# Kernel tuning notes

Measured on AMD Instinct MI355X. Metric: run time of the kernel, lower is better.

Reference implementation:

```python
import jax, jax.numpy as jnp
import numpy as np

B, T, M, P = 512, 64, 256, 256


def setup_inputs() -> dict:
    key = jax.random.key(0)
    ks = jax.random.split(key, 17)
    w = lambda i, shape: (jax.random.normal(ks[i], shape, jnp.float32) * 0.05)
    return {
        "encoded_inputs": jax.random.normal(ks[0], (B, T, M), jnp.float32),
        "y": jax.random.normal(ks[1], (B, T, 1), jnp.float32),
        "tar": jax.random.normal(ks[2], (B, 2), jnp.float32),
        "train": 1,
        "Wd_w": w(3, (M, 2 * P)), "Wd_b": w(4, (M,)),
        "Ud_w": w(5, (M, M)),
        "vd_w": w(6, (1, M)),
        "wt_w": w(7, (1, M + 1)), "wt_b": w(8, (1,)),
        "Wy_w": w(9, (P, P + M)), "Wy_b": w(10, (P,)),
        "vy_w": w(11, (1, P)), "vy_b": w(12, (1,)),
        "Wih": w(13, (4 * P, 1)), "Whh": w(14, (4 * P, P)),
        "bih": w(15, (4 * P,)), "bhh": w(16, (4 * P,)),
    }


def _lstm_cell(x, h, c, Wih, Whh, bih, bhh):
    # torch.nn.LSTMCell gate order: i, f, g, o
    g = x @ Wih.T + h @ Whh.T + (bih + bhh)
    i, f, gg, o = jnp.split(g, 4, axis=1)
    c = jax.nn.sigmoid(f) * c + jax.nn.sigmoid(i) * jnp.tanh(gg)
    h = jax.nn.sigmoid(o) * jnp.tanh(c)
    return h, c


def reference(encoded_inputs, y, tar, train,
              Wd_w, Wd_b, Ud_w, vd_w, wt_w, wt_b,
              Wy_w, Wy_b, vy_w, vy_b, Wih, Whh, bih, bhh):
    Bn = encoded_inputs.shape[0]
    Pn = Whh.shape[1]
    Mn = encoded_inputs.shape[2]
    h0 = jnp.zeros((Bn, Pn), encoded_inputs.dtype)
    c0 = jnp.zeros((Bn, Pn), encoded_inputs.dtype)
    ctx0 = jnp.zeros((Bn, Mn), encoded_inputs.dtype)
    # U_d(encoded_inputs) is loop-invariant
    y1 = jnp.einsum('btm,nm->btn', encoded_inputs, Ud_w)  # (B,T,M)

    def attend(h, s):
        x1 = jnp.concatenate([h, s], axis=1) @ Wd_w.T + Wd_b      # (B,M)
        z1 = jnp.tanh(x1[:, None, :] + y1)                        # (B,T,M)
        l = jnp.einsum('btm,m->bt', z1, vd_w[0])                  # (B,T)
        beta = jax.nn.softmax(l, axis=1)
        return jnp.einsum('bt,btm->bm', beta, encoded_inputs)     # (B,M)

    def step(carry, y_t):
        h, s, _ = carry
        c_t = attend(h, s)
        y_til = jnp.concatenate([c_t, y_t], axis=1) @ wt_w.T + wt_b  # (B,1)
        h, s = _lstm_cell(y_til, h, s, Wih, Whh, bih, bhh)
        return (h, s, c_t), None

    (h, s, c_t), _ = jax.lax.scan(step, (h0, c0, ctx0), jnp.swapaxes(y, 0, 1))

    def head(h):
        return (jnp.concatenate([h, c_t], axis=1) @ Wy_w.T + Wy_b) @ vy_w.T + vy_b

    def extra(h, s, inp):
        y_til = jnp.concatenate([c_t, inp], axis=1) @ wt_w.T + wt_b
        h, s = _lstm_cell(y_til, h, s, Wih, Whh, bih, bhh)
        return h, s, head(h)

    y_Tp1 = head(h)
    if train:
        h, s, y_Tp2 = extra(h, s, tar[:, 0:1])
        h, s, y_Tp3 = extra(h, s, tar[:, 1:2])
    else:
        h, s, y_Tp2 = extra(h, s, y_Tp1)
        h, s, y_Tp3 = extra(h, s, y_Tp2)
    return (y_Tp1, y_Tp2, y_Tp3)
```

## Files before the change

### kernel.cpp

```cpp
#include <hip/hip_runtime.h>


typedef unsigned short u16;
typedef unsigned int u32;
typedef _Float16 half_t;
typedef half_t h2 __attribute__((ext_vector_type(2)));

#define BB 512
#define TT 64
#define MM 256
#define PP 256
#define YS 264
#define ES 68
#define NROW 2
#define NTH 512

#define WD16_OFF  0
#define WHH16_OFF 131072
#define WY16_OFF  393216
#define WQ_ELEMS  524288
#define WQ_BYTES  (WQ_ELEMS * 2)

struct H8 { h2 p[4]; };

#if defined(__has_builtin)
#if __has_builtin(__builtin_amdgcn_fdot2)
#define FDOT2(a, b, c) __builtin_amdgcn_fdot2((a), (b), (c), false)
#endif
#endif
#ifndef FDOT2
__device__ __forceinline__ float FDOT2(h2 a, h2 b, float c) {
  return c + (float)a[0] * (float)b[0] + (float)a[1] * (float)b[1];
}
#endif

__device__ __forceinline__ float dot8(const H8 w, const H8 a, float acc) {
  acc = FDOT2(w.p[0], a.p[0], acc);
  acc = FDOT2(w.p[1], a.p[1], acc);
  acc = FDOT2(w.p[2], a.p[2], acc);
  acc = FDOT2(w.p[3], a.p[3], acc);
  return acc;
}
__device__ __forceinline__ u16 f2h(float f) {
  union { half_t h; u16 u; } x; x.h = (half_t)f; return x.u;
}
__device__ __forceinline__ void unpackH8(const H8 v, float f[8]) {
#pragma unroll
  for (int i = 0; i < 8; ++i) f[i] = (float)v.p[i >> 1][i & 1];
}
__device__ __forceinline__ void ldf8(const float* p, float f[8]) {
  float4 a = *(const float4*)p;
  float4 b = *(const float4*)(p + 4);
  f[0]=a.x; f[1]=a.y; f[2]=a.z; f[3]=a.w;
  f[4]=b.x; f[5]=b.y; f[6]=b.z; f[7]=b.w;
}
__device__ __forceinline__ float tanh_fast(float x) {
  float e = __builtin_amdgcn_exp2f(x * 2.885390081777927f);
  return 1.0f - 2.0f * __builtin_amdgcn_rcpf(1.0f + e);
}
__device__ __forceinline__ float sigmoid_fast(float x) {
  float e = __builtin_amdgcn_exp2f(x * -1.4426950408889634f);
  return __builtin_amdgcn_rcpf(1.0f + e);
}

__global__ __launch_bounds__(256) void prep_kernel(
    const float* __restrict__ Wd, const float* __restrict__ Whh,
    const float* __restrict__ Wy, u16* __restrict__ o) {
  int i = blockIdx.x * 256 + threadIdx.x;
  float v;
  if (i < WHH16_OFF) {
    int ki = i & 7, n = (i >> 3) & 255, kb = i >> 11;
    v = Wd[n * 512 + kb * 8 + ki];
  } else if (i < WY16_OFF) {
    int r = i - WHH16_OFF;
    int ki = r & 7, n = (r >> 3) & 1023, kb = r >> 13;
    v = Whh[n * 256 + kb * 8 + ki];
  } else {
    int r = i - WY16_OFF;
    int ki = r & 7, n = (r >> 3) & 255, kb = r >> 11;
    v = Wy[n * 512 + kb * 8 + ki];
  }
  o[i] = f2h(v);
}

template <int WQ>
__global__ __launch_bounds__(NTH, 2) void scan_kernel(
    const float* __restrict__ E,
    const float* __restrict__ yin,
    const float* __restrict__ tar,
    const int*   __restrict__ train,
    const void*  __restrict__ Wd_q,
    const float* __restrict__ Wd_b,
    const float* __restrict__ Ud_w,
    const float* __restrict__ vd_w,
    const float* __restrict__ wt_w,
    const float* __restrict__ wt_b,
    const void*  __restrict__ Wy_q,
    const float* __restrict__ Wy_b,
    const float* __restrict__ vy_w,
    const float* __restrict__ vy_b,
    const float* __restrict__ Wih,
    const void*  __restrict__ Whh_q,
    const float* __restrict__ bih,
    const float* __restrict__ bhh,
    float* __restrict__ out)
{
  __shared__ __align__(16) u16   y1l[NROW][TT * YS];
  __shared__ __align__(16) u16   e16T[NROW][MM * ES];
  __shared__ __align__(16) u32   hs16[NROW][256];
  __shared__ __align__(16) u32   ctx16p[NROW][128];
  __shared__ __align__(16) float ctx[NROW][MM];
  __shared__ __align__(16) float x1a[NROW][MM];
  __shared__ __align__(16) float x1b[NROW][MM];
  __shared__ __align__(16) float lpart[NROW][4][TT];
  __shared__ __align__(16) u16   betas16[NROW][TT];
  __shared__ __align__(16) float part[10][MM];
  __shared__ float red[8];
  __shared__ float sc[NROW];

  const int j  = threadIdx.x;
  const int n  = j & 255;
  const int kh = j >> 8;
  const int wv = j >> 6;
  const int b0 = blockIdx.x * NROW;

  ((u32*)hs16)[j] = 0;
  float creg0 = 0.f, creg1 = 0.f;

  const float wih0 = Wih[n],       wih1 = Wih[n + 256];
  const float wih2 = Wih[n + 512], wih3 = Wih[n + 768];
  const float bb0 = bih[n]       + bhh[n];
  const float bb1 = bih[n + 256] + bhh[n + 256];
  const float bb2 = bih[n + 512] + bhh[n + 512];
  const float bb3 = bih[n + 768] + bhh[n + 768];
  const float wtM = wt_w[MM], wtb = wt_b[0];

  {
    const float* __restrict__ Eb0 = E + (size_t)b0 * TT * MM;
    for (int i = j; i < NROW * TT * MM; i += NTH) {
      int r = i >> 14;
      int idx = i & 16383;
      int t = idx >> 8, m = idx & 255;
      e16T[r][m * ES + t] = f2h(Eb0[i]);
    }
  }

  {
    const float* __restrict__ Eb = E + (size_t)(b0 + kh) * TT * MM;
    const float* __restrict__ Uj = Ud_w + (size_t)n * MM;
    for (int t0 = 0; t0 < TT; t0 += 16) {
      float acc[16];
#pragma unroll
      for (int i = 0; i < 16; ++i) acc[i] = 0.f;
      for (int m0 = 0; m0 < MM; m0 += 8) {
        float w[8]; ldf8(Uj + m0, w);
#pragma unroll
        for (int tt = 0; tt < 16; ++tt) {
          float e[8]; ldf8(Eb + (size_t)(t0 + tt) * MM + m0, e);
#pragma unroll
          for (int mm = 0; mm < 8; ++mm) acc[tt] = fmaf(e[mm], w[mm], acc[tt]);
        }
      }
#pragma unroll
      for (int tt = 0; tt < 16; ++tt)
        y1l[kh][(t0 + tt) * YS + n] = f2h(acc[tt]);
    }
  }
  __syncthreads();

  auto gates_apply = [&](int r, float g0, float g1, float g2, float g3,
                         float ytil) {
    g0 += ytil * wih0 + bb0;
    g1 += ytil * wih1 + bb1;
    g2 += ytil * wih2 + bb2;
    g3 += ytil * wih3 + bb3;
    float& cr = r ? creg1 : creg0;
    float c = sigmoid_fast(g1) * cr + sigmoid_fast(g0) * tanh_fast(g2);
    float h = sigmoid_fast(g3) * tanh_fast(c);
    cr = c;
    u16* hsu = (u16*)hs16[r];
    hsu[n] = f2h(h);
    hsu[256 + n] = f2h(c);
  };

  auto head_store = [&](int outIdx) {
    float p0 = 0.f, p1 = 0.f;
    if (WQ) {
      const u16* Wy16 = (const u16*)Wy_q;
      const u16* ph = Wy16 + (size_t)((kh * 16) * 256 + n) * 8;
      const u16* pc = Wy16 + (size_t)((32 + kh * 16) * 256 + n) * 8;
      const u32* hb0 = &hs16[0][kh * 64];
      const u32* hb1 = &hs16[1][kh * 64];
      const u32* cb0 = &ctx16p[0][kh * 64];
      const u32* cb1 = &ctx16p[1][kh * 64];
#pragma unroll 4
      for (int kb2 = 0; kb2 < 16; ++kb2) {
        H8 wh = *(const H8*)ph; ph += 2048;
        H8 wc = *(const H8*)pc; pc += 2048;
        H8 hp0 = *(const H8*)&hb0[kb2 * 4];
        H8 hp1 = *(const H8*)&hb1[kb2 * 4];
        H8 cp0 = *(const H8*)&cb0[kb2 * 4];
        H8 cp1 = *(const H8*)&cb1[kb2 * 4];
        p0 = dot8(wh, hp0, p0); p0 = dot8(wc, cp0, p0);
        p1 = dot8(wh, hp1, p1); p1 = dot8(wc, cp1, p1);
      }
    } else {
      const float* W = (const float*)Wy_q + (size_t)n * 512 + kh * 128;
#pragma unroll 2
      for (int kb2 = 0; kb2 < 16; ++kb2) {
        H8 hp0v = *(const H8*)&hs16[0][kh * 64 + kb2 * 4];
        H8 hp1v = *(const H8*)&hs16[1][kh * 64 + kb2 * 4];
        float hf0[8], hf1[8]; unpackH8(hp0v, hf0); unpackH8(hp1v, hf1);
        float ch0[8], ch1[8];
        ldf8(&ctx[0][kh * 128 + kb2 * 8], ch0);
        ldf8(&ctx[1][kh * 128 + kb2 * 8], ch1);
        float wh[8], wc[8];
        ldf8(W + kb2 * 8, wh);
        ldf8(W + 256 + kb2 * 8, wc);
#pragma unroll
        for (int i = 0; i < 8; ++i) {
          p0 = fmaf(hf0[i], wh[i], p0); p0 = fmaf(ch0[i], wc[i], p0);
          p1 = fmaf(hf1[i], wh[i], p1); p1 = fmaf(ch1[i], wc[i], p1);
        }
      }
    }
    if (kh) { part[0][n] = p0; part[1][n] = p1; }
    __syncthreads();
    if (kh == 0) {
      float q0 = (p0 + part[0][n] + Wy_b[n]) * vy_w[n];
      float q1 = (p1 + part[1][n] + Wy_b[n]) * vy_w[n];
#pragma unroll
      for (int off = 32; off; off >>= 1) {
        q0 += __shfl_xor(q0, off, 64);
        q1 += __shfl_xor(q1, off, 64);
      }
      if ((j & 63) == 0) { red[wv] = q0; red[4 + wv] = q1; }
    }
    __syncthreads();
    if (j == 0) {
      float o0 = red[0] + red[1] + red[2] + red[3] + vy_b[0];
      float o1 = red[4] + red[5] + red[6] + red[7] + vy_b[0];
      out[(size_t)outIdx * BB + b0] = o0;
      out[(size_t)outIdx * BB + b0 + 1] = o1;
      sc[0] = o0; sc[1] = o1;
    }
    __syncthreads();
  };

  for (int step = 0; step < TT; ++step) {
    float sg0r0 = 0, sg0r1 = 0, sg1r0 = 0, sg1r1 = 0;
    float sg2r0 = 0, sg2r1 = 0, sg3r0 = 0, sg3r1 = 0;
    {
      float ax0 = 0.f, ax1 = 0.f;
      float g00 = 0, g01 = 0, g10 = 0, g11 = 0;
      float g20 = 0, g21 = 0, g30 = 0, g31 = 0;
      if (WQ) {
        const u16* Wd16 = (const u16*)Wd_q;
        const u16* Wh16 = (const u16*)Whh_q;
        const u16* pdh = Wd16 + (size_t)((kh * 16) * 256 + n) * 8;
        const u16* pdc = Wd16 + (size_t)((32 + kh * 16) * 256 + n) * 8;
        const u16* p0 = Wh16 + (size_t)((kh * 16) * 1024 + n) * 8;
        const u16* p1 = p0 + 256 * 8;
        const u16* p2 = p0 + 512 * 8;
        const u16* p3 = p0 + 768 * 8;
        const u32* hb0 = &hs16[0][kh * 64];
        const u32* hb1 = &hs16[1][kh * 64];
        const u32* cb0 = &hs16[0][128 + kh * 64];
        const u32* cb1 = &hs16[1][128 + kh * 64];
#pragma unroll 4
        for (int kb2 = 0; kb2 < 16; ++kb2) {
          H8 hp0 = *(const H8*)&hb0[kb2 * 4];
          H8 hp1 = *(const H8*)&hb1[kb2 * 4];
          H8 cp0 = *(const H8*)&cb0[kb2 * 4];
          H8 cp1 = *(const H8*)&cb1[kb2 * 4];
          H8 wdh = *(const H8*)pdh; pdh += 2048;
          H8 wdc = *(const H8*)pdc; pdc += 2048;
          H8 w0 = *(const H8*)p0; p0 += 8192;
          H8 w1 = *(const H8*)p1; p1 += 8192;
          H8 w2 = *(const H8*)p2; p2 += 8192;
          H8 w3 = *(const H8*)p3; p3 += 8192;
          ax0 = dot8(wdh, hp0, ax0); ax0 = dot8(wdc, cp0, ax0);
          ax1 = dot8(wdh, hp1, ax1); ax1 = dot8(wdc, cp1, ax1);
          g00 = dot8(w0, hp0, g00); g01 = dot8(w0, hp1, g01);
          g10 = dot8(w1, hp0, g10); g11 = dot8(w1, hp1, g11);
          g20 = dot8(w2, hp0, g20); g21 = dot8(w2, hp1, g21);
          g30 = dot8(w3, hp0, g30); g31 = dot8(w3, hp1, g31);
        }
      } else {
        const float* wdp = (const float*)Wd_q + (size_t)n * 512 + kh * 128;
        const float* w0p = (const float*)Whh_q + (size_t)n * 256 + kh * 128;
#pragma unroll 2
        for (int kb2 = 0; kb2 < 16; ++kb2) {
          H8 hp0v = *(const H8*)&hs16[0][kh * 64 + kb2 * 4];
          H8 hp1v = *(const H8*)&hs16[1][kh * 64 + kb2 * 4];
          H8 cp0v = *(const H8*)&hs16[0][128 + kh * 64 + kb2 * 4];
          H8 cp1v = *(const H8*)&hs16[1][128 + kh * 64 + kb2 * 4];
          float hf0[8], hf1[8], cf0[8], cf1[8];
          unpackH8(hp0v, hf0); unpackH8(hp1v, hf1);
          unpackH8(cp0v, cf0); unpackH8(cp1v, cf1);
          float wh[8], wc[8], w0[8], w1[8], w2[8], w3[8];
          ldf8(wdp + kb2 * 8, wh);
          ldf8(wdp + 256 + kb2 * 8, wc);
          ldf8(w0p + kb2 * 8, w0);
          ldf8(w0p + 256 * 256 + kb2 * 8, w1);
          ldf8(w0p + 512 * 256 + kb2 * 8, w2);
          ldf8(w0p + 768 * 256 + kb2 * 8, w3);
#pragma unroll
          for (int i = 0; i < 8; ++i) {
            ax0 = fmaf(hf0[i], wh[i], ax0); ax0 = fmaf(cf0[i], wc[i], ax0);
            ax1 = fmaf(hf1[i], wh[i], ax1); ax1 = fmaf(cf1[i], wc[i], ax1);
            g00 = fmaf(hf0[i], w0[i], g00); g01 = fmaf(hf1[i], w0[i], g01);
            g10 = fmaf(hf0[i], w1[i], g10); g11 = fmaf(hf1[i], w1[i], g11);
            g20 = fmaf(hf0[i], w2[i], g20); g21 = fmaf(hf1[i], w2[i], g21);
            g30 = fmaf(hf0[i], w3[i], g30); g31 = fmaf(hf1[i], w3[i], g31);
          }
        }
      }
      if (kh) {
        x1b[0][n] = ax0; x1b[1][n] = ax1;
        part[2][n] = g00; part[3][n] = g01;
        part[4][n] = g10; part[5][n] = g11;
        part[6][n] = g20; part[7][n] = g21;
        part[8][n] = g30; part[9][n] = g31;
      } else {
        float bia = Wd_b[n];
        x1a[0][n] = ax0 + bia; x1a[1][n] = ax1 + bia;
        sg0r0 = g00; sg0r1 = g01; sg1r0 = g10; sg1r1 = g11;
        sg2r0 = g20; sg2r1 = g21; sg3r0 = g30; sg3r1 = g31;
      }
    }
    __syncthreads();

    {
      const int q = (j >> 6) & 3, tq = j & 63;
      const u16* __restrict__ yrow = &y1l[kh][tq * YS + q * 64];
      const float* __restrict__ xap = &x1a[kh][q * 64];
      const float* __restrict__ xbp = &x1b[kh][q * 64];
      const float* __restrict__ vp = vd_w + q * 64;
      float lp = 0.f;
#pragma unroll 2
      for (int m0 = 0; m0 < 64; m0 += 8) {
        H8 yv = *(const H8*)(yrow + m0);
        float yf[8]; unpackH8(yv, yf);
        float xf[8]; ldf8(xap + m0, xf);
        float xg[8]; ldf8(xbp + m0, xg);
        float vf[8]; ldf8(vp + m0, vf);
#pragma unroll
        for (int mm = 0; mm < 8; ++mm) {
          float z = tanh_fast(xf[mm] + xg[mm] + yf[mm]);
          lp = fmaf(z, vf[mm], lp);
        }
      }
      lpart[kh][q][tq] = lp;
    }
    __syncthreads();

    if (n < 64) {
      const int t = n;
      float l = lpart[kh][0][t] + lpart[kh][1][t] + lpart[kh][2][t] +
                lpart[kh][3][t];
      float mx = l;
#pragma unroll
      for (int off = 32; off; off >>= 1) mx = fmaxf(mx, __shfl_xor(mx, off, 64));
      float e = __builtin_amdgcn_exp2f((l - mx) * 1.4426950408889634f);
      float sm = e;
#pragma unroll
      for (int off = 32; off; off >>= 1) sm += __shfl_xor(sm, off, 64);
      betas16[kh][t] = f2h(e * __builtin_amdgcn_rcpf(sm));
    }
    __syncthreads();

    {
      const u16* __restrict__ ep = &e16T[kh][n * ES];
      float acc = 0.f;
#pragma unroll
      for (int t0 = 0; t0 < TT; t0 += 8) {
        h2 e0 = *(const h2*)(ep + t0);
        h2 e1 = *(const h2*)(ep + t0 + 2);
        h2 e2 = *(const h2*)(ep + t0 + 4);
        h2 e3 = *(const h2*)(ep + t0 + 6);
        H8 bp = *(const H8*)&betas16[kh][t0];
        acc = FDOT2(bp.p[0], e0, acc);
        acc = FDOT2(bp.p[1], e1, acc);
        acc = FDOT2(bp.p[2], e2, acc);
        acc = FDOT2(bp.p[3], e3, acc);
      }
      ctx[kh][n] = acc;
      ((u16*)ctx16p[kh])[n] = f2h(acc);
      float p = acc * wt_w[n];
#pragma unroll
      for (int off = 32; off; off >>= 1) p += __shfl_xor(p, off, 64);
      if ((j & 63) == 0) red[wv] = p;
    }
    __syncthreads();

    if (kh == 0) {
      float yt0 = red[0] + red[1] + red[2] + red[3] +
                  yin[(size_t)b0 * TT + step] * wtM + wtb;
      float yt1 = red[4] + red[5] + red[6] + red[7] +
                  yin[(size_t)(b0 + 1) * TT + step] * wtM + wtb;
      gates_apply(0, sg0r0 + part[2][n], sg1r0 + part[4][n],
                  sg2r0 + part[6][n], sg3r0 + part[8][n], yt0);
      gates_apply(1, sg0r1 + part[3][n], sg1r1 + part[5][n],
                  sg2r1 + part[7][n], sg3r1 + part[9][n], yt1);
    }
    __syncthreads();
  }

  {
    float p = ctx[kh][n] * wt_w[n];
#pragma unroll
    for (int off = 32; off; off >>= 1) p += __shfl_xor(p, off, 64);
    if ((j & 63) == 0) red[wv] = p;
  }
  __syncthreads();
  const float ctdot0 = red[0] + red[1] + red[2] + red[3];
  const float ctdot1 = red[4] + red[5] + red[6] + red[7];

  head_store(0);

  const int tr = train[0];
  for (int e = 0; e < 2; ++e) {
    float g00 = 0, g01 = 0, g10 = 0, g11 = 0;
    float g20 = 0, g21 = 0, g30 = 0, g31 = 0;
    if (WQ) {
      const u16* Wh16 = (const u16*)Whh_q;
      const u16* p0 = Wh16 + (size_t)((kh * 16) * 1024 + n) * 8;
      const u16* p1 = p0 + 256 * 8;
      const u16* p2 = p0 + 512 * 8;
      const u16* p3 = p0 + 768 * 8;
      const u32* hb0 = &hs16[0][kh * 64];
      const u32* hb1 = &hs16[1][kh * 64];
#pragma unroll 4
      for (int kb2 = 0; kb2 < 16; ++kb2) {
        H8 hp0 = *(const H8*)&hb0[kb2 * 4];
        H8 hp1 = *(const H8*)&hb1[kb2 * 4];
        H8 w0 = *(const H8*)p0; p0 += 8192;
        H8 w1 = *(const H8*)p1; p1 += 8192;
        H8 w2 = *(const H8*)p2; p2 += 8192;
        H8 w3 = *(const H8*)p3; p3 += 8192;
        g00 = dot8(w0, hp0, g00); g01 = dot8(w0, hp1, g01);
        g10 = dot8(w1, hp0, g10); g11 = dot8(w1, hp1, g11);
        g20 = dot8(w2, hp0, g20); g21 = dot8(w2, hp1, g21);
        g30 = dot8(w3, hp0, g30); g31 = dot8(w3, hp1, g31);
      }
    } else {
      const float* w0p = (const float*)Whh_q + (size_t)n * 256 + kh * 128;
#pragma unroll 2
      for (int kb2 = 0; kb2 < 16; ++kb2) {
        H8 hp0v = *(const H8*)&hs16[0][kh * 64 + kb2 * 4];
        H8 hp1v = *(const H8*)&hs16[1][kh * 64 + kb2 * 4];
        float hf0[8], hf1[8]; unpackH8(hp0v, hf0); unpackH8(hp1v, hf1);
        float w0[8], w1[8], w2[8], w3[8];
        ldf8(w0p + kb2 * 8, w0);
        ldf8(w0p + 256 * 256 + kb2 * 8, w1);
        ldf8(w0p + 512 * 256 + kb2 * 8, w2);
        ldf8(w0p + 768 * 256 + kb2 * 8, w3);
#pragma unroll
        for (int i = 0; i < 8; ++i) {
          g00 = fmaf(hf0[i], w0[i], g00); g01 = fmaf(hf1[i], w0[i], g01);
          g10 = fmaf(hf0[i], w1[i], g10); g11 = fmaf(hf1[i], w1[i], g11);
          g20 = fmaf(hf0[i], w2[i], g20); g21 = fmaf(hf1[i], w2[i], g21);
          g30 = fmaf(hf0[i], w3[i], g30); g31 = fmaf(hf1[i], w3[i], g31);
        }
      }
    }
    if (kh) {
      part[2][n] = g00; part[3][n] = g01;
      part[4][n] = g10; part[5][n] = g11;
      part[6][n] = g20; part[7][n] = g21;
      part[8][n] = g30; part[9][n] = g31;
    }
    __syncthreads();
    if (kh == 0) {
      float inp0 = tr ? tar[(size_t)b0 * 2 + e] : sc[0];
      float inp1 = tr ? tar[(size_t)(b0 + 1) * 2 + e] : sc[1];
      float yt0 = ctdot0 + inp0 * wtM + wtb;
      float yt1 = ctdot1 + inp1 * wtM + wtb;
      gates_apply(0, g00 + part[2][n], g10 + part[4][n],
                  g20 + part[6][n], g30 + part[8][n], yt0);
      gates_apply(1, g01 + part[3][n], g11 + part[5][n],
                  g21 + part[7][n], g31 + part[9][n], yt1);
    }
    __syncthreads();
    head_store(1 + e);
  }
}

extern "C" void kernel_launch(void* const* d_in, const int* in_sizes, int n_in,
                              void* d_out, int out_size, void* d_ws, size_t ws_size,
                              hipStream_t stream) {
  const float* E     = (const float*)d_in[0];
  const float* yin   = (const float*)d_in[1];
  const float* tar   = (const float*)d_in[2];
  const int*   train = (const int*)d_in[3];
  const float* Wd_w  = (const float*)d_in[4];
  const float* Wd_b  = (const float*)d_in[5];
  const float* Ud_w  = (const float*)d_in[6];
  const float* vd_w  = (const float*)d_in[7];
  const float* wt_w  = (const float*)d_in[8];
  const float* wt_b  = (const float*)d_in[9];
  const float* Wy_w  = (const float*)d_in[10];
  const float* Wy_b  = (const float*)d_in[11];
  const float* vy_w  = (const float*)d_in[12];
  const float* vy_b  = (const float*)d_in[13];
  const float* Wih   = (const float*)d_in[14];
  const float* Whh   = (const float*)d_in[15];
  const float* bih   = (const float*)d_in[16];
  const float* bhh   = (const float*)d_in[17];

  float* out = (float*)d_out;

  if (ws_size >= (size_t)WQ_BYTES) {
    u16* wq = (u16*)d_ws;
    prep_kernel<<<dim3(WQ_ELEMS / 256), dim3(256), 0, stream>>>(
        Wd_w, Whh, Wy_w, wq);
    scan_kernel<1><<<dim3(BB / NROW), dim3(NTH), 0, stream>>>(
        E, yin, tar, train, wq + WD16_OFF, Wd_b, Ud_w, vd_w, wt_w, wt_b,
        wq + WY16_OFF, Wy_b, vy_w, vy_b, Wih, wq + WHH16_OFF, bih, bhh, out);
  } else {
    scan_kernel<0><<<dim3(BB / NROW), dim3(NTH), 0, stream>>>(
        E, yin, tar, train, Wd_w, Wd_b, Ud_w, vd_w, wt_w, wt_b,
        Wy_w, Wy_b, vy_w, vy_b, Wih, Whh, bih, bhh, out);
  }

  (void)in_sizes; (void)n_in; (void)out_size;
}
```

Baseline: 1.101 ms.

## Double block threads to 1024 and repartition recurrent matvec, attention across four groups

Raises the block to 1024 threads and splits the per-step work across four 256-thread groups. Groups 0-1 each take half of K for the i/f/g gate rows, while groups 2-3 take the Wd attention projection plus the o-gate rows. Attention scoring, softmax and context are spread over the extra threads, and y inputs are staged in shared memory. The aim is shorter per-step latency in the sequential 64-step scan, at the cost of higher register pressure from launch_bounds(1024,4), more partial-sum traffic, and the fp32 ctx now being taken from its fp16 copy.

Measured after the change: 1.087 ms. No clear change (-1.2%).

```diff
diff --git a/kernel.cpp b/kernel.cpp
--- a/kernel.cpp
+++ b/kernel.cpp
@@ -13,7 +13,7 @@
 #define YS 264
 #define ES 68
 #define NROW 2
-#define NTH 512
+#define NTH 1024
 
 #define WD16_OFF  0
 #define WHH16_OFF 131072
@@ -43,6 +43,9 @@
 }
 __device__ __forceinline__ u16 f2h(float f) {
   union { half_t h; u16 u; } x; x.h = (half_t)f; return x.u;
+}
+__device__ __forceinline__ float h2f(u16 u) {
+  union { u16 u; half_t h; } x; x.u = u; return (float)x.h;
 }
 __device__ __forceinline__ void unpackH8(const H8 v, float f[8]) {
 #pragma unroll
@@ -84,7 +87,7 @@
 }
 
 template <int WQ>
-__global__ __launch_bounds__(NTH, 2) void scan_kernel(
+__global__ __launch_bounds__(NTH, 4) void scan_kernel(
     const float* __restrict__ E,
     const float* __restrict__ yin,
     const float* __restrict__ tar,
@@ -109,22 +112,22 @@
   __shared__ __align__(16) u16   e16T[NROW][MM * ES];
   __shared__ __align__(16) u32   hs16[NROW][256];
   __shared__ __align__(16) u32   ctx16p[NROW][128];
-  __shared__ __align__(16) float ctx[NROW][MM];
-  __shared__ __align__(16) float x1a[NROW][MM];
-  __shared__ __align__(16) float x1b[NROW][MM];
-  __shared__ __align__(16) float lpart[NROW][4][TT];
+  __shared__ __align__(16) float px1[4][MM];
+  __shared__ __align__(16) float pg[6][MM];
+  __shared__ __align__(16) float pg3[4][MM];
+  __shared__ __align__(16) float lpart[NROW][8][TT];
   __shared__ __align__(16) u16   betas16[NROW][TT];
-  __shared__ __align__(16) float part[10][MM];
-  __shared__ float red[8];
+  __shared__ __align__(16) float ysh[NROW][TT];
+  __shared__ float red[16];
   __shared__ float sc[NROW];
 
-  const int j  = threadIdx.x;
-  const int n  = j & 255;
-  const int kh = j >> 8;
-  const int wv = j >> 6;
-  const int b0 = blockIdx.x * NROW;
-
-  ((u32*)hs16)[j] = 0;
+  const int j   = threadIdx.x;
+  const int n   = j & 255;
+  const int grp = j >> 8;
+  const int wv  = j >> 6;
+  const int b0  = blockIdx.x * NROW;
+
+  if (j < 512) ((u32*)hs16)[j] = 0;
   float creg0 = 0.f, creg1 = 0.f;
 
   const float wih0 = Wih[n],       wih1 = Wih[n + 256];
@@ -135,6 +138,9 @@
   const float bb3 = bih[n + 768] + bhh[n + 768];
   const float wtM = wt_w[MM], wtb = wt_b[0];
 
+  if (j < NROW * TT)
+    ysh[j >> 6][j & 63] = yin[(size_t)(b0 + (j >> 6)) * TT + (j & 63)];
+
   {
     const float* __restrict__ Eb0 = E + (size_t)b0 * TT * MM;
     for (int i = j; i < NROW * TT * MM; i += NTH) {
@@ -146,9 +152,10 @@
   }
 
   {
-    const float* __restrict__ Eb = E + (size_t)(b0 + kh) * TT * MM;
+    const int rs = grp >> 1, ths = grp & 1;
+    const float* __restrict__ Eb = E + (size_t)(b0 + rs) * TT * MM;
     const float* __restrict__ Uj = Ud_w + (size_t)n * MM;
-    for (int t0 = 0; t0 < TT; t0 += 16) {
+    for (int t0 = ths * 32; t0 < ths * 32 + 32; t0 += 16) {
       float acc[16];
 #pragma unroll
       for (int i = 0; i < 16; ++i) acc[i] = 0.f;
@@ -163,20 +170,20 @@
       }
 #pragma unroll
       for (int tt = 0; tt < 16; ++tt)
-        y1l[kh][(t0 + tt) * YS + n] = f2h(acc[tt]);
+        y1l[rs][(t0 + tt) * YS + n] = f2h(acc[tt]);
     }
   }
   __syncthreads();
 
-  auto gates_apply = [&](int r, float g0, float g1, float g2, float g3,
+  auto gates_apply = [&](int r, float gi, float gf, float gg, float go,
                          float ytil) {
-    g0 += ytil * wih0 + bb0;
-    g1 += ytil * wih1 + bb1;
-    g2 += ytil * wih2 + bb2;
-    g3 += ytil * wih3 + bb3;
+    gi += ytil * wih0 + bb0;
+    gf += ytil * wih1 + bb1;
+    gg += ytil * wih2 + bb2;
+    go += ytil * wih3 + bb3;
     float& cr = r ? creg1 : creg0;
-    float c = sigmoid_fast(g1) * cr + sigmoid_fast(g0) * tanh_fast(g2);
-    float h = sigmoid_fast(g3) * tanh_fast(c);
+    float c = sigmoid_fast(gf) * cr + sigmoid_fast(gi) * tanh_fast(gg);
+    float h = sigmoid_fast(go) * tanh_fast(c);
     cr = c;
     u16* hsu = (u16*)hs16[r];
     hsu[n] = f2h(h);
@@ -184,62 +191,44 @@
   };
 
   auto head_store = [&](int outIdx) {
-    float p0 = 0.f, p1 = 0.f;
+    float p = 0.f;
+    const int rr = grp >> 1, seg = grp & 1;
+    const u32* st = seg ? ctx16p[rr] : hs16[rr];
     if (WQ) {
-      const u16* Wy16 = (const u16*)Wy_q;
-      const u16* ph = Wy16 + (size_t)((kh * 16) * 256 + n) * 8;
-      const u16* pc = Wy16 + (size_t)((32 + kh * 16) * 256 + n) * 8;
-      const u32* hb0 = &hs16[0][kh * 64];
-      const u32* hb1 = &hs16[1][kh * 64];
-      const u32* cb0 = &ctx16p[0][kh * 64];
-      const u32* cb1 = &ctx16p[1][kh * 64];
-#pragma unroll 4
-      for (int kb2 = 0; kb2 < 16; ++kb2) {
-        H8 wh = *(const H8*)ph; ph += 2048;
-        H8 wc = *(const H8*)pc; pc += 2048;
-        H8 hp0 = *(const H8*)&hb0[kb2 * 4];
-        H8 hp1 = *(const H8*)&hb1[kb2 * 4];
-        H8 cp0 = *(const H8*)&cb0[kb2 * 4];
-        H8 cp1 = *(const H8*)&cb1[kb2 * 4];
-        p0 = dot8(wh, hp0, p0); p0 = dot8(wc, cp0, p0);
-        p1 = dot8(wh, hp1, p1); p1 = dot8(wc, cp1, p1);
+      const u16* pw = (const u16*)Wy_q + ((size_t)(seg * 32) * 256 + n) * 8;
+#pragma unroll 2
+      for (int kb = 0; kb < 32; ++kb) {
+        H8 w = *(const H8*)pw; pw += 2048;
+        H8 s = *(const H8*)&st[kb * 4];
+        p = dot8(w, s, p);
       }
     } else {
-      const float* W = (const float*)Wy_q + (size_t)n * 512 + kh * 128;
-#pragma unroll 2
-      for (int kb2 = 0; kb2 < 16; ++kb2) {
-        H8 hp0v = *(const H8*)&hs16[0][kh * 64 + kb2 * 4];
-        H8 hp1v = *(const H8*)&hs16[1][kh * 64 + kb2 * 4];
-        float hf0[8], hf1[8]; unpackH8(hp0v, hf0); unpackH8(hp1v, hf1);
-        float ch0[8], ch1[8];
-        ldf8(&ctx[0][kh * 128 + kb2 * 8], ch0);
-        ldf8(&ctx[1][kh * 128 + kb2 * 8], ch1);
-        float wh[8], wc[8];
-        ldf8(W + kb2 * 8, wh);
-        ldf8(W + 256 + kb2 * 8, wc);
-#pragma unroll
-        for (int i = 0; i < 8; ++i) {
-          p0 = fmaf(hf0[i], wh[i], p0); p0 = fmaf(ch0[i], wc[i], p0);
-          p1 = fmaf(hf1[i], wh[i], p1); p1 = fmaf(ch1[i], wc[i], p1);
-        }
-      }
-    }
-    if (kh) { part[0][n] = p0; part[1][n] = p1; }
-    __syncthreads();
-    if (kh == 0) {
-      float q0 = (p0 + part[0][n] + Wy_b[n]) * vy_w[n];
-      float q1 = (p1 + part[1][n] + Wy_b[n]) * vy_w[n];
+      const float* W = (const float*)Wy_q + (size_t)n * 512 + seg * 256;
+#pragma unroll 2
+      for (int kb = 0; kb < 32; ++kb) {
+        H8 sv = *(const H8*)&st[kb * 4];
+        float sf[8]; unpackH8(sv, sf);
+        float w[8]; ldf8(W + kb * 8, w);
+#pragma unroll
+        for (int i = 0; i < 8; ++i) p = fmaf(sf[i], w[i], p);
+      }
+    }
+    if (grp) px1[grp - 1][n] = p;
+    __syncthreads();
+    if (grp == 0) {
+      float q0 = (p + px1[0][n] + Wy_b[n]) * vy_w[n];
+      float q1 = (px1[1][n] + px1[2][n] + Wy_b[n]) * vy_w[n];
 #pragma unroll
       for (int off = 32; off; off >>= 1) {
         q0 += __shfl_xor(q0, off, 64);
         q1 += __shfl_xor(q1, off, 64);
       }
-      if ((j & 63) == 0) { red[wv] = q0; red[4 + wv] = q1; }
+      if ((j & 63) == 0) { red[wv] = q0; red[8 + wv] = q1; }
     }
     __syncthreads();
     if (j == 0) {
       float o0 = red[0] + red[1] + red[2] + red[3] + vy_b[0];
-      float o1 = red[4] + red[5] + red[6] + red[7] + vy_b[0];
+      float o1 = red[8] + red[9] + red[10] + red[11] + vy_b[0];
       out[(size_t)outIdx * BB + b0] = o0;
       out[(size_t)outIdx * BB + b0 + 1] = o1;
       sc[0] = o0; sc[1] = o1;
@@ -247,103 +236,211 @@
     __syncthreads();
   };
 
+  auto mv4 = [&](float& m0, float& m1, float& m2, float& m3, float& m4,
+                 float& m5) {
+    m0 = m1 = m2 = m3 = m4 = m5 = 0.f;
+    if (WQ) {
+      const u16* Whh16 = (const u16*)Whh_q;
+      if (grp < 2) {
+        const int kb0 = grp << 4;
+        const u16* pw = Whh16 + ((size_t)kb0 * 1024 + n) * 8;
+#pragma unroll 2
+        for (int kb2 = 0; kb2 < 16; ++kb2) {
+          const int kb = kb0 + kb2;
+          H8 h0 = *(const H8*)&hs16[0][kb * 4];
+          H8 h1 = *(const H8*)&hs16[1][kb * 4];
+          H8 w0 = *(const H8*)pw;
+          H8 w1 = *(const H8*)(pw + 2048);
+          H8 w2 = *(const H8*)(pw + 4096);
+          pw += 8192;
+          m0 = dot8(w0, h0, m0); m1 = dot8(w0, h1, m1);
+          m2 = dot8(w1, h0, m2); m3 = dot8(w1, h1, m3);
+          m4 = dot8(w2, h0, m4); m5 = dot8(w2, h1, m5);
+        }
+      } else {
+        const int half = grp - 2;
+        const u16* p3 = Whh16 + ((size_t)(half * 16) * 1024 + 768 + n) * 8;
+#pragma unroll 2
+        for (int kb2 = 0; kb2 < 16; ++kb2) {
+          const int kg = half * 16 + kb2;
+          H8 w3 = *(const H8*)p3; p3 += 8192;
+          H8 h0 = *(const H8*)&hs16[0][kg * 4];
+          H8 h1 = *(const H8*)&hs16[1][kg * 4];
+          m0 = dot8(w3, h0, m0); m1 = dot8(w3, h1, m1);
+        }
+      }
+    } else {
+      const float* Whf = (const float*)Whh_q;
+      if (grp < 2) {
+        const int kb0 = grp << 4;
+        const float* pw0 = Whf + (size_t)n * 256 + kb0 * 8;
+        const float* pw1 = pw0 + 256 * 256;
+        const float* pw2 = pw0 + 512 * 256;
+#pragma unroll 2
+        for (int kb2 = 0; kb2 < 16; ++kb2) {
+          const int kb = kb0 + kb2;
+          H8 h0v = *(const H8*)&hs16[0][kb * 4];
+          H8 h1v = *(const H8*)&hs16[1][kb * 4];
+          float hf0[8], hf1[8]; unpackH8(h0v, hf0); unpackH8(h1v, hf1);
+          float w0[8], w1[8], w2[8];
+          ldf8(pw0 + kb2 * 8, w0);
+          ldf8(pw1 + kb2 * 8, w1);
+          ldf8(pw2 + kb2 * 8, w2);
+#pragma unroll
+          for (int i = 0; i < 8; ++i) {
+            m0 = fmaf(hf0[i], w0[i], m0); m1 = fmaf(hf1[i], w0[i], m1);
+            m2 = fmaf(hf0[i], w1[i], m2); m3 = fmaf(hf1[i], w1[i], m3);
+            m4 = fmaf(hf0[i], w2[i], m4); m5 = fmaf(hf1[i], w2[i], m5);
+          }
+        }
+      } else {
+        const int half = grp - 2;
+        const float* p3f = Whf + ((size_t)(768 + n)) * 256 + half * 128;
+#pragma unroll 2
+        for (int kb2 = 0; kb2 < 16; ++kb2) {
+          const int kg = half * 16 + kb2;
+          H8 h0v = *(const H8*)&hs16[0][kg * 4];
+          H8 h1v = *(const H8*)&hs16[1][kg * 4];
+          float hf0[8], hf1[8]; unpackH8(h0v, hf0); unpackH8(h1v, hf1);
+          float w3[8]; ldf8(p3f + kb2 * 8, w3);
+#pragma unroll
+          for (int i = 0; i < 8; ++i) {
+            m0 = fmaf(hf0[i], w3[i], m0); m1 = fmaf(hf1[i], w3[i], m1);
+          }
+        }
+      }
+    }
+  };
+
   for (int step = 0; step < TT; ++step) {
-    float sg0r0 = 0, sg0r1 = 0, sg1r0 = 0, sg1r1 = 0;
-    float sg2r0 = 0, sg2r1 = 0, sg3r0 = 0, sg3r1 = 0;
+    float s0 = 0.f, s1 = 0.f, s2 = 0.f, s3 = 0.f, s4 = 0.f, s5 = 0.f;
     {
-      float ax0 = 0.f, ax1 = 0.f;
-      float g00 = 0, g01 = 0, g10 = 0, g11 = 0;
-      float g20 = 0, g21 = 0, g30 = 0, g31 = 0;
+      float a0 = 0, a1 = 0, a2 = 0, a3 = 0, a4 = 0, a5 = 0;
       if (WQ) {
-        const u16* Wd16 = (const u16*)Wd_q;
-        const u16* Wh16 = (const u16*)Whh_q;
-        const u16* pdh = Wd16 + (size_t)((kh * 16) * 256 + n) * 8;
-        const u16* pdc = Wd16 + (size_t)((32 + kh * 16) * 256 + n) * 8;
-        const u16* p0 = Wh16 + (size_t)((kh * 16) * 1024 + n) * 8;
-        const u16* p1 = p0 + 256 * 8;
-        const u16* p2 = p0 + 512 * 8;
-        const u16* p3 = p0 + 768 * 8;
-        const u32* hb0 = &hs16[0][kh * 64];
-        const u32* hb1 = &hs16[1][kh * 64];
-        const u32* cb0 = &hs16[0][128 + kh * 64];
-        const u32* cb1 = &hs16[1][128 + kh * 64];
-#pragma unroll 4
-        for (int kb2 = 0; kb2 < 16; ++kb2) {
-          H8 hp0 = *(const H8*)&hb0[kb2 * 4];
-          H8 hp1 = *(const H8*)&hb1[kb2 * 4];
-          H8 cp0 = *(const H8*)&cb0[kb2 * 4];
-          H8 cp1 = *(const H8*)&cb1[kb2 * 4];
-          H8 wdh = *(const H8*)pdh; pdh += 2048;
-          H8 wdc = *(const H8*)pdc; pdc += 2048;
-          H8 w0 = *(const H8*)p0; p0 += 8192;
-          H8 w1 = *(const H8*)p1; p1 += 8192;
-          H8 w2 = *(const H8*)p2; p2 += 8192;
-          H8 w3 = *(const H8*)p3; p3 += 8192;
-          ax0 = dot8(wdh, hp0, ax0); ax0 = dot8(wdc, cp0, ax0);
-          ax1 = dot8(wdh, hp1, ax1); ax1 = dot8(wdc, cp1, ax1);
-          g00 = dot8(w0, hp0, g00); g01 = dot8(w0, hp1, g01);
-          g10 = dot8(w1, hp0, g10); g11 = dot8(w1, hp1, g11);
-          g20 = dot8(w2, hp0, g20); g21 = dot8(w2, hp1, g21);
-          g30 = dot8(w3, hp0, g30); g31 = dot8(w3, hp1, g31);
+        const u16* Whh16 = (const u16*)Whh_q;
+        if (grp < 2) {
+          const int kb0 = grp << 4;
+          const u16* pw = Whh16 + ((size_t)kb0 * 1024 + n) * 8;
+#pragma unroll 2
+          for (int kb2 = 0; kb2 < 16; ++kb2) {
+            const int kb = kb0 + kb2;
+            H8 h0 = *(const H8*)&hs16[0][kb * 4];
+            H8 h1 = *(const H8*)&hs16[1][kb * 4];
+            H8 w0 = *(const H8*)pw;
+            H8 w1 = *(const H8*)(pw + 2048);
+            H8 w2 = *(const H8*)(pw + 4096);
+            pw += 8192;
+            a0 = dot8(w0, h0, a0); a1 = dot8(w0, h1, a1);
+            a2 = dot8(w1, h0, a2); a3 = dot8(w1, h1, a3);
+            a4 = dot8(w2, h0, a4); a5 = dot8(w2, h1, a5);
+          }
+        } else {
+          const int half = grp - 2;
+          const u16* pd = (const u16*)Wd_q + ((size_t)(half * 32) * 256 + n) * 8;
+          const u16* p3 = Whh16 + ((size_t)(half * 16) * 1024 + 768 + n) * 8;
+#pragma unroll 2
+          for (int kb2 = 0; kb2 < 16; ++kb2) {
+            const int kd = half * 32 + kb2 * 2;
+            const int kg = half * 16 + kb2;
+            H8 s00 = *(const H8*)&hs16[0][kd * 4];
+            H8 s01 = *(const H8*)&hs16[0][kd * 4 + 4];
+            H8 s10 = *(const H8*)&hs16[1][kd * 4];
+            H8 s11 = *(const H8*)&hs16[1][kd * 4 + 4];
+            H8 wd0 = *(const H8*)pd;
+            H8 wd1 = *(const H8*)(pd + 2048);
+            pd += 4096;
+            H8 w3 = *(const H8*)p3; p3 += 8192;
+            H8 h0 = *(const H8*)&hs16[0][kg * 4];
+            H8 h1 = *(const H8*)&hs16[1][kg * 4];
+            a0 = dot8(wd0, s00, a0); a0 = dot8(wd1, s01, a0);
+            a1 = dot8(wd0, s10, a1); a1 = dot8(wd1, s11, a1);
+            a2 = dot8(w3, h0, a2);   a3 = dot8(w3, h1, a3);
+          }
         }
       } else {
-        const float* wdp = (const float*)Wd_q + (size_t)n * 512 + kh * 128;
-        const float* w0p = (const float*)Whh_q + (size_t)n * 256 + kh * 128;
-#pragma unroll 2
-        for (int kb2 = 0; kb2 < 16; ++kb2) {
-          H8 hp0v = *(const H8*)&hs16[0][kh * 64 + kb2 * 4];
-          H8 hp1v = *(const H8*)&hs16[1][kh * 64 + kb2 * 4];
-          H8 cp0v = *(const H8*)&hs16[0][128 + kh * 64 + kb2 * 4];
-          H8 cp1v = *(const H8*)&hs16[1][128 + kh * 64 + kb2 * 4];
-          float hf0[8], hf1[8], cf0[8], cf1[8];
-          unpackH8(hp0v, hf0); unpackH8(hp1v, hf1);
-          unpackH8(cp0v, cf0); unpackH8(cp1v, cf1);
-          float wh[8], wc[8], w0[8], w1[8], w2[8], w3[8];
-          ldf8(wdp + kb2 * 8, wh);
-          ldf8(wdp + 256 + kb2 * 8, wc);
-          ldf8(w0p + kb2 * 8, w0);
-          ldf8(w0p + 256 * 256 + kb2 * 8, w1);
-          ldf8(w0p + 512 * 256 + kb2 * 8, w2);
-          ldf8(w0p + 768 * 256 + kb2 * 8, w3);
-#pragma unroll
-          for (int i = 0; i < 8; ++i) {
-            ax0 = fmaf(hf0[i], wh[i], ax0); ax0 = fmaf(cf0[i], wc[i], ax0);
-            ax1 = fmaf(hf1[i], wh[i], ax1); ax1 = fmaf(cf1[i], wc[i], ax1);
-            g00 = fmaf(hf0[i], w0[i], g00); g01 = fmaf(hf1[i], w0[i], g01);
-            g10 = fmaf(hf0[i], w1[i], g10); g11 = fmaf(hf1[i], w1[i], g11);
-            g20 = fmaf(hf0[i], w2[i], g20); g21 = fmaf(hf1[i], w2[i], g21);
-            g30 = fmaf(hf0[i], w3[i], g30); g31 = fmaf(hf1[i], w3[i], g31);
+        const float* Whf = (const float*)Whh_q;
+        if (grp < 2) {
+          const int kb0 = grp << 4;
+          const float* pw0 = Whf + (size_t)n * 256 + kb0 * 8;
+          const float* pw1 = pw0 + 256 * 256;
+          const float* pw2 = pw0 + 512 * 256;
+#pragma unroll 2
+          for (int kb2 = 0; kb2 < 16; ++kb2) {
+            const int kb = kb0 + kb2;
+            H8 h0v = *(const H8*)&hs16[0][kb * 4];
+            H8 h1v = *(const H8*)&hs16[1][kb * 4];
+            float hf0[8], hf1[8]; unpackH8(h0v, hf0); unpackH8(h1v, hf1);
+            float w0[8], w1[8], w2[8];
+            ldf8(pw0 + kb2 * 8, w0);
+            ldf8(pw1 + kb2 * 8, w1);
+            ldf8(pw2 + kb2 * 8, w2);
+#pragma unroll
+            for (int i = 0; i < 8; ++i) {
+              a0 = fmaf(hf0[i], w0[i], a0); a1 = fmaf(hf1[i], w0[i], a1);
+              a2 = fmaf(hf0[i], w1[i], a2); a3 = fmaf(hf1[i], w1[i], a3);
+              a4 = fmaf(hf0[i], w2[i], a4); a5 = fmaf(hf1[i], w2[i], a5);
+            }
           }
-        }
-      }
-      if (kh) {
-        x1b[0][n] = ax0; x1b[1][n] = ax1;
-        part[2][n] = g00; part[3][n] = g01;
-        part[4][n] = g10; part[5][n] = g11;
-        part[6][n] = g20; part[7][n] = g21;
-        part[8][n] = g30; part[9][n] = g31;
+        } else {
+          const int half = grp - 2;
+          const float* Wdf = (const float*)Wd_q + (size_t)n * 512 + half * 256;
+          const float* p3f = Whf + ((size_t)(768 + n)) * 256 + half * 128;
+#pragma unroll 2
+          for (int kb2 = 0; kb2 < 16; ++kb2) {
+            const int kd = half * 32 + kb2 * 2;
+            const int kg = half * 16 + kb2;
+            H8 s00v = *(const H8*)&hs16[0][kd * 4];
+            H8 s01v = *(const H8*)&hs16[0][kd * 4 + 4];
+            H8 s10v = *(const H8*)&hs16[1][kd * 4];
+            H8 s11v = *(const H8*)&hs16[1][kd * 4 + 4];
+            float f00[8], f01[8], f10[8], f11[8];
+            unpackH8(s00v, f00); unpackH8(s01v, f01);
+            unpackH8(s10v, f10); unpackH8(s11v, f11);
+            H8 h0v = *(const H8*)&hs16[0][kg * 4];
+            H8 h1v = *(const H8*)&hs16[1][kg * 4];
+            float hf0[8], hf1[8]; unpackH8(h0v, hf0); unpackH8(h1v, hf1);
+            float wd0[8], wd1[8], w3[8];
+            ldf8(Wdf + kb2 * 16, wd0);
+            ldf8(Wdf + kb2 * 16 + 8, wd1);
+            ldf8(p3f + kb2 * 8, w3);
+#pragma unroll
+            for (int i = 0; i < 8; ++i) {
+              a0 = fmaf(f00[i], wd0[i], a0); a0 = fmaf(f01[i], wd1[i], a0);
+              a1 = fmaf(f10[i], wd0[i], a1); a1 = fmaf(f11[i], wd1[i], a1);
+              a2 = fmaf(hf0[i], w3[i], a2);  a3 = fmaf(hf1[i], w3[i], a3);
+            }
+          }
+        }
+      }
+      if (grp == 0) {
+        s0 = a0; s1 = a1; s2 = a2; s3 = a3; s4 = a4; s5 = a5;
+      } else if (grp == 1) {
+        pg[0][n] = a0; pg[1][n] = a1; pg[2][n] = a2;
+        pg[3][n] = a3; pg[4][n] = a4; pg[5][n] = a5;
+      } else if (grp == 2) {
+        float bia = Wd_b[n];
+        px1[0][n] = a0 + bia; px1[1][n] = a1 + bia;
+        pg3[0][n] = a2; pg3[1][n] = a3;
       } else {
-        float bia = Wd_b[n];
-        x1a[0][n] = ax0 + bia; x1a[1][n] = ax1 + bia;
-        sg0r0 = g00; sg0r1 = g01; sg1r0 = g10; sg1r1 = g11;
-        sg2r0 = g20; sg2r1 = g21; sg3r0 = g30; sg3r1 = g31;
+        px1[2][n] = a0; px1[3][n] = a1;
+        pg3[2][n] = a2; pg3[3][n] = a3;
       }
     }
     __syncthreads();
 
     {
-      const int q = (j >> 6) & 3, tq = j & 63;
-      const u16* __restrict__ yrow = &y1l[kh][tq * YS + q * 64];
-      const float* __restrict__ xap = &x1a[kh][q * 64];
-      const float* __restrict__ xbp = &x1b[kh][q * 64];
-      const float* __restrict__ vp = vd_w + q * 64;
+      const int r = j >> 9, e8 = (j >> 6) & 7, t = j & 63;
+      const u16* __restrict__ yrow = &y1l[r][t * YS + e8 * 32];
+      const float* __restrict__ xh = &px1[r][e8 * 32];
+      const float* __restrict__ xc = &px1[2 + r][e8 * 32];
+      const float* __restrict__ vp = vd_w + e8 * 32;
       float lp = 0.f;
-#pragma unroll 2
-      for (int m0 = 0; m0 < 64; m0 += 8) {
+#pragma unroll
+      for (int m0 = 0; m0 < 32; m0 += 8) {
         H8 yv = *(const H8*)(yrow + m0);
         float yf[8]; unpackH8(yv, yf);
-        float xf[8]; ldf8(xap + m0, xf);
-        float xg[8]; ldf8(xbp + m0, xg);
+        float xf[8]; ldf8(xh + m0, xf);
+        float xg[8]; ldf8(xc + m0, xg);
         float vf[8]; ldf8(vp + m0, vf);
 #pragma unroll
         for (int mm = 0; mm < 8; ++mm) {
@@ -351,14 +448,15 @@
           lp = fmaf(z, vf[mm], lp);
         }
       }
-      lpart[kh][q][tq] = lp;
-    }
-    __syncthreads();
-
-    if (n < 64) {
-      const int t = n;
-      float l = lpart[kh][0][t] + lpart[kh][1][t] + lpart[kh][2][t] +
-                lpart[kh][3][t];
+      lpart[r][e8][t] = lp;
+    }
+    __syncthreads();
+
+    if ((j & 511) < 64) {
+      const int r = j >> 9, t = j & 63;
+      float l = lpart[r][0][t] + lpart[r][1][t] + lpart[r][2][t] +
+                lpart[r][3][t] + lpart[r][4][t] + lpart[r][5][t] +
+                lpart[r][6][t] + lpart[r][7][t];
       float mx = l;
 #pragma unroll
       for (int off = 32; off; off >>= 1) mx = fmaxf(mx, __shfl_xor(mx, off, 64));
@@ -366,12 +464,13 @@
       float sm = e;
 #pragma unroll
       for (int off = 32; off; off >>= 1) sm += __shfl_xor(sm, off, 64);
-      betas16[kh][t] = f2h(e * __builtin_amdgcn_rcpf(sm));
-    }
-    __syncthreads();
-
-    {
-      const u16* __restrict__ ep = &e16T[kh][n * ES];
+      betas16[r][t] = f2h(e * __builtin_amdgcn_rcpf(sm));
+    }
+    __syncthreads();
+
+    if (((j >> 8) & 1) == 0) {
+      const int r = j >> 9;
+      const u16* __restrict__ ep = &e16T[r][n * ES];
       float acc = 0.f;
 #pragma unroll
       for (int t0 = 0; t0 < TT; t0 += 8) {
@@ -379,14 +478,13 @@
         h2 e1 = *(const h2*)(ep + t0 + 2);
         h2 e2 = *(const h2*)(ep + t0 + 4);
         h2 e3 = *(const h2*)(ep + t0 + 6);
-        H8 bp = *(const H8*)&betas16[kh][t0];
+        H8 bp = *(const H8*)&betas16[r][t0];
         acc = FDOT2(bp.p[0], e0, acc);
         acc = FDOT2(bp.p[1], e1, acc);
         acc = FDOT2(bp.p[2], e2, acc);
         acc = FDOT2(bp.p[3], e3, acc);
       }
-      ctx[kh][n] = acc;
-      ((u16*)ctx16p[kh])[n] = f2h(acc);
+      ((u16*)ctx16p[r])[n] = f2h(acc);
       float p = acc * wt_w[n];
 #pragma unroll
       for (int off = 32; off; off >>= 1) p += __shfl_xor(p, off, 64);
@@ -394,93 +492,52 @@
     }
     __syncthreads();
 
-    if (kh == 0) {
-      float yt0 = red[0] + red[1] + red[2] + red[3] +
-                  yin[(size_t)b0 * TT + step] * wtM + wtb;
-      float yt1 = red[4] + red[5] + red[6] + red[7] +
-                  yin[(size_t)(b0 + 1) * TT + step] * wtM + wtb;
-      gates_apply(0, sg0r0 + part[2][n], sg1r0 + part[4][n],
-                  sg2r0 + part[6][n], sg3r0 + part[8][n], yt0);
-      gates_apply(1, sg0r1 + part[3][n], sg1r1 + part[5][n],
-                  sg2r1 + part[7][n], sg3r1 + part[9][n], yt1);
-    }
-    __syncthreads();
-  }
-
-  {
-    float p = ctx[kh][n] * wt_w[n];
+    if (grp == 0) {
+      float yt0 = red[0] + red[1] + red[2] + red[3] + ysh[0][step] * wtM + wtb;
+      float yt1 = red[8] + red[9] + red[10] + red[11] + ysh[1][step] * wtM + wtb;
+      gates_apply(0, s0 + pg[0][n], s2 + pg[2][n], s4 + pg[4][n],
+                  pg3[0][n] + pg3[2][n], yt0);
+      gates_apply(1, s1 + pg[1][n], s3 + pg[3][n], s5 + pg[5][n],
+                  pg3[1][n] + pg3[3][n], yt1);
+    }
+    __syncthreads();
+  }
+
+  if (((j >> 8) & 1) == 0) {
+    const int r = j >> 9;
+    float p = h2f(((const u16*)ctx16p[r])[n]) * wt_w[n];
 #pragma unroll
     for (int off = 32; off; off >>= 1) p += __shfl_xor(p, off, 64);
     if ((j & 63) == 0) red[wv] = p;
   }
   __syncthreads();
-  const float ctdot0 = red[0] + red[1] + red[2] + red[3];
-  const float ctdot1 = red[4] + red[5] + red[6] + red[7];
+  const float ctd0 = red[0] + red[1] + red[2] + red[3];
+  const float ctd1 = red[8] + red[9] + red[10] + red[11];
 
   head_store(0);
 
   const int tr = train[0];
   for (int e = 0; e < 2; ++e) {
-    float g00 = 0, g01 = 0, g10 = 0, g11 = 0;
-    float g20 = 0, g21 = 0, g30 = 0, g31 = 0;
-    if (WQ) {
-      const u16* Wh16 = (const u16*)Whh_q;
-      const u16* p0 = Wh16 + (size_t)((kh * 16) * 1024 + n) * 8;
-      const u16* p1 = p0 + 256 * 8;
-      const u16* p2 = p0 + 512 * 8;
-      const u16* p3 = p0 + 768 * 8;
-      const u32* hb0 = &hs16[0][kh * 64];
-      const u32* hb1 = &hs16[1][kh * 64];
-#pragma unroll 4
-      for (int kb2 = 0; kb2 < 16; ++kb2) {
-        H8 hp0 = *(const H8*)&hb0[kb2 * 4];
-        H8 hp1 = *(const H8*)&hb1[kb2 * 4];
-        H8 w0 = *(const H8*)p0; p0 += 8192;
-        H8 w1 = *(const H8*)p1; p1 += 8192;
-        H8 w2 = *(const H8*)p2; p2 += 8192;
-        H8 w3 = *(const H8*)p3; p3 += 8192;
-        g00 = dot8(w0, hp0, g00); g01 = dot8(w0, hp1, g01);
-        g10 = dot8(w1, hp0, g10); g11 = dot8(w1, hp1, g11);
-        g20 = dot8(w2, hp0, g20); g21 = dot8(w2, hp1, g21);
-        g30 = dot8(w3, hp0, g30); g31 = dot8(w3, hp1, g31);
-      }
-    } else {
-      const float* w0p = (const float*)Whh_q + (size_t)n * 256 + kh * 128;
-#pragma unroll 2
-      for (int kb2 = 0; kb2 < 16; ++kb2) {
-        H8 hp0v = *(const H8*)&hs16[0][kh * 64 + kb2 * 4];
-        H8 hp1v = *(const H8*)&hs16[1][kh * 64 + kb2 * 4];
-        float hf0[8], hf1[8]; unpackH8(hp0v, hf0); unpackH8(hp1v, hf1);
-        float w0[8], w1[8], w2[8], w3[8];
-        ldf8(w0p + kb2 * 8, w0);
-        ldf8(w0p + 256 * 256 + kb2 * 8, w1);
-        ldf8(w0p + 512 * 256 + kb2 * 8, w2);
-        ldf8(w0p + 768 * 256 + kb2 * 8, w3);
-#pragma unroll
-        for (int i = 0; i < 8; ++i) {
-          g00 = fmaf(hf0[i], w0[i], g00); g01 = fmaf(hf1[i], w0[i], g01);
-          g10 = fmaf(hf0[i], w1[i], g10); g11 = fmaf(hf1[i], w1[i], g11);
-          g20 = fmaf(hf0[i], w2[i], g20); g21 = fmaf(hf1[i], w2[i], g21);
-          g30 = fmaf(hf0[i], w3[i], g30); g31 = fmaf(hf1[i], w3[i], g31);
-        }
-      }
-    }
-    if (kh) {
-      part[2][n] = g00; part[3][n] = g01;
-      part[4][n] = g10; part[5][n] = g11;
-      part[6][n] = g20; part[7][n] = g21;
-      part[8][n] = g30; part[9][n] = g31;
-    }
-    __syncthreads();
-    if (kh == 0) {
+    float m0, m1, m2, m3, m4, m5;
+    mv4(m0, m1, m2, m3, m4, m5);
+    if (grp == 1) {
+      pg[0][n] = m0; pg[1][n] = m1; pg[2][n] = m2;
+      pg[3][n] = m3; pg[4][n] = m4; pg[5][n] = m5;
+    } else if (grp == 2) {
+      pg3[0][n] = m0; pg3[1][n] = m1;
+    } else if (grp == 3) {
+      pg3[2][n] = m0; pg3[3][n] = m1;
+    }
+    __syncthreads();
+    if (grp == 0) {
       float inp0 = tr ? tar[(size_t)b0 * 2 + e] : sc[0];
       float inp1 = tr ? tar[(size_t)(b0 + 1) * 2 + e] : sc[1];
-      float yt0 = ctdot0 + inp0 * wtM + wtb;
-      float yt1 = ctdot1 + inp1 * wtM + wtb;
-      gates_apply(0, g00 + part[2][n], g10 + part[4][n],
-                  g20 + part[6][n], g30 + part[8][n], yt0);
-      gates_apply(1, g01 + part[3][n], g11 + part[5][n],
-                  g21 + part[7][n], g31 + part[9][n], yt1);
+      float yt0 = ctd0 + inp0 * wtM + wtb;
+      float yt1 = ctd1 + inp1 * wtM + wtb;
+      gates_apply(0, m0 + pg[0][n], m2 + pg[2][n], m4 + pg[4][n],
+                  pg3[0][n] + pg3[2][n], yt0);
+      gates_apply(1, m1 + pg[1][n], m3 + pg[3][n], m5 + pg[5][n],
+                  pg3[1][n] + pg3[3][n], yt1);
     }
     __syncthreads();
     head_store(1 + e);
```
